# Performance work log

Measured on AMD Instinct MI355X. Metric: run time of the kernel, lower is better.

The kernel has to match this reference:

```python
import jax, jax.numpy as jnp
import numpy as np

NUM_INTERVALS = 12
DOMAIN_MIN = -10.0
DOMAIN_MAX = 0.0


def _build_pla_coeffs(num_intervals=NUM_INTERVALS, dmin=DOMAIN_MIN, dmax=DOMAIN_MAX):
    """Least-squares linear fit of exp(x) on each interval (matches np.polyfit in source)."""
    xs = np.linspace(dmin, dmax, 1001)
    ys = np.exp(xs)
    edges = np.linspace(dmin, dmax, num_intervals + 1)
    ms, cs = [], []
    for i in range(num_intervals):
        mask = (xs >= edges[i]) & (xs <= edges[i + 1])
        m, c = np.polyfit(xs[mask], ys[mask], 1)
        ms.append(m)
        cs.append(c)
    # 'intervals' buffer in source stores only the LOWER edge of each interval (len = num_intervals)
    return (np.asarray(ms, np.float32), np.asarray(cs, np.float32), edges[:num_intervals].astype(np.float32))


def setup_inputs() -> dict:
    key = jax.random.key(0)
    scores = jax.random.normal(key, (8, 12, 512, 512), dtype=jnp.float32)
    m_np, c_np, a_np = _build_pla_coeffs()
    return {
        "scores": scores,
        "coeffs_m": jnp.asarray(m_np),
        "coeffs_c": jnp.asarray(c_np),
        "intervals": jnp.asarray(a_np),
    }


def reference(scores, coeffs_m, coeffs_c, intervals):
    # 1) stable shift by row max
    max_scores = jnp.max(scores, axis=-1, keepdims=True)
    shifted = scores - max_scores

    # 2) snap to Q32.26 fixed point
    fp_scale = 2.0 ** 26
    fx = jnp.clip(jnp.round(shifted * fp_scale), -(2.0 ** 31), 2.0 ** 31 - 1) / fp_scale

    # 3) piecewise-linear exp: bucket search against interval lower edges + coeff gather
    xc = jnp.clip(fx, DOMAIN_MIN, DOMAIN_MAX)
    # sum(x >= a_i) == searchsorted(a, x, side='right'); original clamps idx to len(intervals)-2
    idx = jnp.clip(jnp.searchsorted(intervals, xc, side="right") - 1, 0, intervals.shape[0] - 2)
    exps = coeffs_m[idx] * xc + coeffs_c[idx]

    # 4) normalize
    softmax_out = exps / (jnp.sum(exps, axis=-1, keepdims=True) + 1e-9)

    # 5) per-tensor symmetric INT8 fake-quant (STE form; same forward value)
    qmax = 127.0
    scale = jnp.maximum(jnp.max(jnp.abs(softmax_out)) / qmax, 1e-8)
    q = jnp.clip(jnp.round(softmax_out / scale), -qmax, qmax) * scale
    return softmax_out + jax.lax.stop_gradient(q - softmax_out)
```

## Files before the change

### kernel.cpp

```cpp
#include <hip/hip_runtime.h>

#define THREADS 256
#define WPB 4
#define ROW_LEN 512

typedef float f4 __attribute__((ext_vector_type(4)));
typedef char  c8 __attribute__((ext_vector_type(8)));

__device__ __forceinline__ float wave_reduce_max(float v) {
#pragma unroll
    for (int o = 32; o > 0; o >>= 1) v = fmaxf(v, __shfl_xor(v, o));
    return v;
}
__device__ __forceinline__ float wave_reduce_sum(float v) {
#pragma unroll
    for (int o = 32; o > 0; o >>= 1) v += __shfl_xor(v, o);
    return v;
}

__global__ __launch_bounds__(THREADS) void pla_pass0(
    const float* __restrict__ scores,
    const float* __restrict__ coeffs_m,
    const float* __restrict__ coeffs_c,
    const float* __restrict__ intervals,
    char* __restrict__ svq,
    float* __restrict__ rowg,
    float* __restrict__ slots,
    int nrows)
{
    __shared__ float2 s_mc[12];
    __shared__ float  s_bm[WPB];

    const int tid = threadIdx.x;
    if (tid < 12) s_mc[tid] = make_float2(coeffs_m[tid], coeffs_c[tid]);
    if (tid < WPB) s_bm[tid] = 0.0f;
    __syncthreads();

    const int wave = tid >> 6;
    const int lane = tid & 63;
    const int row  = blockIdx.x * WPB + wave;

    if (row < nrows) {
        float aedge[11];
#pragma unroll
        for (int i = 0; i < 11; ++i) aedge[i] = intervals[i + 1];
        const float c10 = coeffs_c[10];

        const float4* rp = reinterpret_cast<const float4*>(scores + (size_t)row * ROW_LEN);
        float4 v0 = rp[lane];
        float4 v1 = rp[lane + 64];
        float x[8] = {v0.x, v0.y, v0.z, v0.w, v1.x, v1.y, v1.z, v1.w};

        float mx = fmaxf(fmaxf(fmaxf(x[0], x[1]), fmaxf(x[2], x[3])),
                         fmaxf(fmaxf(x[4], x[5]), fmaxf(x[6], x[7])));
        mx = wave_reduce_max(mx);

        float e[8];
        float sum = 0.0f;
#pragma unroll
        for (int j = 0; j < 8; ++j) {
            float sh = x[j] - mx;
            float t = rintf(sh * 67108864.0f);
            t = fminf(fmaxf(t, -2147483648.0f), 2147483648.0f);
            float fx = t * 1.4901161193847656e-8f;
            float xc = fminf(fmaxf(fx, -10.0f), 0.0f);
            int cnt = 0;
#pragma unroll
            for (int i = 0; i < 11; ++i) cnt += (xc >= aedge[i]) ? 1 : 0;
            int idx = min(cnt, 10);
            float2 p = s_mc[idx];
            float ev = p.x * xc + p.y;
            e[j] = ev;
            sum += ev;
        }
        sum = wave_reduce_sum(sum);
        const float inv = 1.0f / (sum + 1e-9f);
        const float k0  = 127.0f / c10;

        c8 q;
#pragma unroll
        for (int j = 0; j < 8; ++j) q[j] = (char)(int)rintf(e[j] * k0);
        c8* qp = reinterpret_cast<c8*>(svq + (size_t)row * ROW_LEN);
        qp[lane] = q;

        if (lane == 0) {
            const float g = c10 * inv * (1.0f / 127.0f);
            rowg[row] = g;
            s_bm[wave] = c10 * inv;
        }
    }
    __syncthreads();
    if (tid == 0) {
        float bm = fmaxf(fmaxf(s_bm[0], s_bm[1]), fmaxf(s_bm[2], s_bm[3]));
        slots[blockIdx.x] = bm;
    }
}

__global__ __launch_bounds__(1024) void reduce_max_kernel(
    const float* __restrict__ slots, float* __restrict__ gmax, int n)
{
    __shared__ float s_w[16];
    const int tid = threadIdx.x;
    float m = 0.0f;
    for (int i = tid; i < n; i += 1024) m = fmaxf(m, slots[i]);
    m = wave_reduce_max(m);
    if ((tid & 63) == 0) s_w[tid >> 6] = m;
    __syncthreads();
    if (tid < 64) {
        float v = (tid < 16) ? s_w[tid] : 0.0f;
        v = wave_reduce_max(v);
        if (tid == 0) gmax[0] = v;
    }
}

__global__ __launch_bounds__(THREADS) void pla_pass1(
    const char* __restrict__ svq,
    const float* __restrict__ rowg,
    const float* __restrict__ gmax,
    float* __restrict__ out,
    int nrows)
{
    const int wave = threadIdx.x >> 6;
    const int lane = threadIdx.x & 63;
    const int row  = blockIdx.x * WPB + wave;
    if (row >= nrows) return;

    const float am     = *gmax;
    const float scale  = fmaxf(am * (1.0f / 127.0f), 1e-8f);
    const float iscale = 1.0f / scale;
    const float f      = rowg[row] * iscale;

    const c8* qp = reinterpret_cast<const c8*>(svq + (size_t)row * ROW_LEN);
    c8 a = qp[lane];

    float o[8];
#pragma unroll
    for (int j = 0; j < 8; ++j) {
        float q = fminf(fmaxf(rintf((float)a[j] * f), -127.0f), 127.0f);
        o[j] = q * scale;
    }
    f4* op = reinterpret_cast<f4*>(out + (size_t)row * ROW_LEN);
    f4 w0 = {o[0], o[1], o[2], o[3]};
    f4 w1 = {o[4], o[5], o[6], o[7]};
    __builtin_nontemporal_store(w0, op + lane);
    __builtin_nontemporal_store(w1, op + lane + 64);
}

extern "C" void kernel_launch(void* const* d_in, const int* in_sizes, int n_in,
                              void* d_out, int out_size, void* d_ws, size_t ws_size,
                              hipStream_t stream) {
    const float* scores    = (const float*)d_in[0];
    const float* coeffs_m  = (const float*)d_in[1];
    const float* coeffs_c  = (const float*)d_in[2];
    const float* intervals = (const float*)d_in[3];
    float* out = (float*)d_out;

    const int nrows  = in_sizes[0] / ROW_LEN;
    const int blocks = (nrows + WPB - 1) / WPB;

    float* slots = (float*)d_ws;
    float* gmax  = (float*)((char*)d_ws + (64 << 10));
    float* rowg  = (float*)((char*)d_ws + (128 << 10));
    char*  svq   = (char*)d_ws + (1 << 20);

    pla_pass0<<<blocks, THREADS, 0, stream>>>(
        scores, coeffs_m, coeffs_c, intervals, svq, rowg, slots, nrows);
    reduce_max_kernel<<<1, 1024, 0, stream>>>(slots, gmax, blocks);
    pla_pass1<<<blocks, THREADS, 0, stream>>>(svq, rowg, gmax, out, nrows);
}
```

Measured before the change: 57.74 us.

## Replace global-max reduce kernel with striped atomicMax slots read in pass1

```diff
diff --git a/kernel.cpp b/kernel.cpp
--- a/kernel.cpp
+++ b/kernel.cpp
@@ -3,6 +3,8 @@
 #define THREADS 256
 #define WPB 4
 #define ROW_LEN 512
+#define NSLOTS 64
+#define SLOT_STRIDE 32
 
 typedef float f4 __attribute__((ext_vector_type(4)));
 typedef char  c8 __attribute__((ext_vector_type(8)));
@@ -25,7 +27,7 @@
     const float* __restrict__ intervals,
     char* __restrict__ svq,
     float* __restrict__ rowg,
-    float* __restrict__ slots,
+    unsigned* __restrict__ slots,
     int nrows)
 {
     __shared__ float2 s_mc[12];
@@ -61,9 +63,8 @@
         for (int j = 0; j < 8; ++j) {
             float sh = x[j] - mx;
             float t = rintf(sh * 67108864.0f);
-            t = fminf(fmaxf(t, -2147483648.0f), 2147483648.0f);
             float fx = t * 1.4901161193847656e-8f;
-            float xc = fminf(fmaxf(fx, -10.0f), 0.0f);
+            float xc = fmaxf(fx, -10.0f);
             int cnt = 0;
 #pragma unroll
             for (int i = 0; i < 11; ++i) cnt += (xc >= aedge[i]) ? 1 : 0;
@@ -84,39 +85,22 @@
         qp[lane] = q;
 
         if (lane == 0) {
-            const float g = c10 * inv * (1.0f / 127.0f);
-            rowg[row] = g;
+            rowg[row]  = c10 * inv * (1.0f / 127.0f);
             s_bm[wave] = c10 * inv;
         }
     }
     __syncthreads();
     if (tid == 0) {
         float bm = fmaxf(fmaxf(s_bm[0], s_bm[1]), fmaxf(s_bm[2], s_bm[3]));
-        slots[blockIdx.x] = bm;
-    }
-}
-
-__global__ __launch_bounds__(1024) void reduce_max_kernel(
-    const float* __restrict__ slots, float* __restrict__ gmax, int n)
-{
-    __shared__ float s_w[16];
-    const int tid = threadIdx.x;
-    float m = 0.0f;
-    for (int i = tid; i < n; i += 1024) m = fmaxf(m, slots[i]);
-    m = wave_reduce_max(m);
-    if ((tid & 63) == 0) s_w[tid >> 6] = m;
-    __syncthreads();
-    if (tid < 64) {
-        float v = (tid < 16) ? s_w[tid] : 0.0f;
-        v = wave_reduce_max(v);
-        if (tid == 0) gmax[0] = v;
+        atomicMax(&slots[(blockIdx.x & (NSLOTS - 1)) * SLOT_STRIDE],
+                  __float_as_uint(bm));
     }
 }
 
 __global__ __launch_bounds__(THREADS) void pla_pass1(
     const char* __restrict__ svq,
     const float* __restrict__ rowg,
-    const float* __restrict__ gmax,
+    const unsigned* __restrict__ slots,
     float* __restrict__ out,
     int nrows)
 {
@@ -125,7 +109,9 @@
     const int row  = blockIdx.x * WPB + wave;
     if (row >= nrows) return;
 
-    const float am     = *gmax;
+    float am = __uint_as_float(slots[lane * SLOT_STRIDE]);
+    am = wave_reduce_max(am);
+
     const float scale  = fmaxf(am * (1.0f / 127.0f), 1e-8f);
     const float iscale = 1.0f / scale;
     const float f      = rowg[row] * iscale;
@@ -158,13 +144,13 @@
     const int nrows  = in_sizes[0] / ROW_LEN;
     const int blocks = (nrows + WPB - 1) / WPB;
 
-    float* slots = (float*)d_ws;
-    float* gmax  = (float*)((char*)d_ws + (64 << 10));
-    float* rowg  = (float*)((char*)d_ws + (128 << 10));
-    char*  svq   = (char*)d_ws + (1 << 20);
+    unsigned* slots = (unsigned*)d_ws;
+    float*    rowg  = (float*)((char*)d_ws + (128 << 10));
+    char*     svq   = (char*)d_ws + (1 << 20);
+
+    hipMemsetAsync(d_ws, 0, NSLOTS * SLOT_STRIDE * sizeof(unsigned), stream);
 
     pla_pass0<<<blocks, THREADS, 0, stream>>>(
         scores, coeffs_m, coeffs_c, intervals, svq, rowg, slots, nrows);
-    reduce_max_kernel<<<1, 1024, 0, stream>>>(slots, gmax, blocks);
-    pla_pass1<<<blocks, THREADS, 0, stream>>>(svq, rowg, gmax, out, nrows);
+    pla_pass1<<<blocks, THREADS, 0, stream>>>(svq, rowg, slots, out, nrows);
 }
```

New measurement: 59.56 us. 1.03x slower.
